# Optimization experiments

Measured on AMD Instinct MI355X. Metric: run time of the kernel, lower is better.

## Reference

```python
import jax, jax.numpy as jnp
import numpy as np


def setup_inputs() -> dict:
    key = jax.random.key(0)
    k1, k2, k3, k4 = jax.random.split(key, 4)
    B, T, C, H = 8, 2048, 1024, 64
    x = jax.random.normal(k1, (B, T, C), dtype=jnp.float32)
    # nn.Linear weights, stored as (in, out) for x @ W
    Wk = jax.random.normal(k2, (C, H), dtype=jnp.float32) * (C ** -0.5)
    Wq = jax.random.normal(k3, (C, H), dtype=jnp.float32) * (C ** -0.5)
    Wv = jax.random.normal(k4, (C, H), dtype=jnp.float32) * (C ** -0.5)
    return {"x": x, "Wk": Wk, "Wq": Wq, "Wv": Wv}


def reference(x, Wk, Wq, Wv):
    B, T, C = x.shape
    k = x @ Wk  # [B,T,H]
    q = x @ Wq  # [B,T,H]
    v = x @ Wv  # [B,T,H]
    # NOTE: original scales by C**-0.5 (full embed dim), not head_size**-0.5
    wei = jnp.einsum("bth,bsh->bts", q, k) * (C ** -0.5)  # [B,T,T]
    causal = jnp.tril(jnp.ones((T, T), dtype=bool))
    wei = jnp.where(causal, wei, -jnp.inf)
    wei = jax.nn.softmax(wei, axis=-1)
    # dropout is identity in eval/reference mode
    out = jnp.einsum("bts,bsh->bth", wei, v)  # [B,T,H]
    return out
```

## Files before the change

### kernel.cpp

```cpp
#include <hip/hip_runtime.h>
#include <hip/hip_bf16.h>
#include <math.h>

#define B_ 8
#define T_ 2048
#define C_ 1024
#define H_ 64
#define M_ (B_*T_)

typedef __attribute__((ext_vector_type(8))) short short8;
typedef __attribute__((ext_vector_type(4))) float f32x4;
typedef unsigned int u32;

__device__ __forceinline__ unsigned short f2bf(float f) {
    u32 u = __builtin_bit_cast(u32, f);
    u += 0x7FFFu + ((u >> 16) & 1u);
    return (unsigned short)(u >> 16);
}
__device__ __forceinline__ float bf2f(unsigned short h) {
    u32 u = ((u32)h) << 16;
    return __builtin_bit_cast(float, u);
}

__device__ __forceinline__ void gl2lds16(const void* g, void* l) {
    __builtin_amdgcn_global_load_lds(
        (const __attribute__((address_space(1))) u32*)g,
        (__attribute__((address_space(3))) u32*)l, 16, 0, 0);
}

__global__ __launch_bounds__(256) void wconv(
    const float* __restrict__ Wk, const float* __restrict__ Wq,
    const float* __restrict__ Wv, unsigned short* __restrict__ wb)
{
    __shared__ unsigned short lt[64][64];
    const int mat = blockIdx.x >> 4;
    const int k0  = (blockIdx.x & 15) * 64;
    const float* src = (mat == 0) ? Wk : (mat == 1 ? Wq : Wv);
    const float sc = (mat == 1) ? 0.03125f : 1.0f;
    const int tid = threadIdx.x;

    for (int it = 0; it < 16; ++it) {
        int idx = it * 256 + tid;
        int r = idx >> 6, cn = idx & 63;
        lt[cn][r] = f2bf(src[(size_t)(k0 + r) * H_ + cn] * sc);
    }
    __syncthreads();
    for (int g = 0; g < 2; ++g) {
        int n  = g * 32 + (tid >> 3);
        int kp = tid & 7;
        int ng = mat * 64 + n;
        short8 v = *reinterpret_cast<const short8*>(&lt[n][kp * 8]);
        char* dst = (char*)wb + (size_t)ng * 2048 + (k0 >> 6) * 128
                  + ((kp * 16) ^ ((ng & 7) << 4));
        *reinterpret_cast<short8*>(dst) = v;
    }
}

#define LOADX(R0,R1,R2,R3,t) {                                        \
    const float* p_ = xrow + (t) * 64;                                \
    R0 = *reinterpret_cast<const float4*>(p_);                        \
    R1 = *reinterpret_cast<const float4*>(p_ + 4);                    \
    R2 = *reinterpret_cast<const float4*>(p_ + 32);                   \
    R3 = *reinterpret_cast<const float4*>(p_ + 36); }

#define STAGEW(buf, t) {                                              \
    _Pragma("unroll") for (int p_ = 0; p_ < 6; ++p_) {                \
        int c_ = p_ * 256 + tid;                                      \
        gl2lds16((const char*)wb + (size_t)(c_ >> 3) * 2048           \
                     + (size_t)(t) * 128 + (c_ & 7) * 16,             \
                 (char*)&Ws[buf][0] + c_ * 16);                       \
    } }

__global__ __launch_bounds__(256) void qkv_mm(
    const float* __restrict__ x, const unsigned short* __restrict__ wb,
    unsigned short* __restrict__ kb, unsigned short* __restrict__ qb,
    unsigned short* __restrict__ vT)
{
    __shared__ __align__(16) unsigned short Ws[2][192 * 64];

    const int tid  = threadIdx.x;
    const int wid  = tid >> 6;
    const int lane = tid & 63;
    const int lr   = lane & 15;
    const int lg   = lane >> 4;
    const int m0   = blockIdx.x * 64;

    const float* xrow = x + (size_t)(m0 + wid * 16 + lr) * C_ + lg * 8;

    f32x4 acc[12];
    #pragma unroll
    for (int c = 0; c < 12; ++c) acc[c] = (f32x4){0.f, 0.f, 0.f, 0.f};

    float4 xA0, xA1, xA2, xA3, xB0, xB1, xB2, xB3, xC0, xC1, xC2, xC3;

    LOADX(xA0, xA1, xA2, xA3, 0);
    __builtin_amdgcn_sched_barrier(0);
    STAGEW(0, 0);
    __builtin_amdgcn_sched_barrier(0);
    LOADX(xB0, xB1, xB2, xB3, 1);
    __builtin_amdgcn_sched_barrier(0);

    #pragma unroll
    for (int t = 0; t < 16; ++t) {
        if (t < 15) asm volatile("s_waitcnt vmcnt(4) lgkmcnt(0)" ::: "memory");
        else        asm volatile("s_waitcnt vmcnt(0) lgkmcnt(0)" ::: "memory");
        __builtin_amdgcn_s_barrier();
        __builtin_amdgcn_sched_barrier(0);
        if (t < 15) { STAGEW((t + 1) & 1, t + 1); }
        __builtin_amdgcn_sched_barrier(0);
        if (t < 14) { LOADX(xC0, xC1, xC2, xC3, t + 2); }
        __builtin_amdgcn_sched_barrier(0);

        short8 af0, af1;
        af0[0] = (short)f2bf(xA0.x); af0[1] = (short)f2bf(xA0.y);
        af0[2] = (short)f2bf(xA0.z); af0[3] = (short)f2bf(xA0.w);
        af0[4] = (short)f2bf(xA1.x); af0[5] = (short)f2bf(xA1.y);
        af0[6] = (short)f2bf(xA1.z); af0[7] = (short)f2bf(xA1.w);
        af1[0] = (short)f2bf(xA2.x); af1[1] = (short)f2bf(xA2.y);
        af1[2] = (short)f2bf(xA2.z); af1[3] = (short)f2bf(xA2.w);
        af1[4] = (short)f2bf(xA3.x); af1[5] = (short)f2bf(xA3.y);
        af1[6] = (short)f2bf(xA3.z); af1[7] = (short)f2bf(xA3.w);

        const char* wbuf = (const char*)&Ws[t & 1][0];
        #pragma unroll
        for (int kc = 0; kc < 2; ++kc) {
            short8 afc = kc ? af1 : af0;
            #pragma unroll
            for (int ct = 0; ct < 12; ++ct) {
                int n = ct * 16 + lr;
                short8 bf = *reinterpret_cast<const short8*>(
                    wbuf + n * 128 + ((kc * 64 + lg * 16) ^ ((n & 7) << 4)));
                acc[ct] = __builtin_amdgcn_mfma_f32_16x16x32_bf16(afc, bf, acc[ct], 0, 0, 0);
            }
        }
        xA0 = xB0; xA1 = xB1; xA2 = xB2; xA3 = xB3;
        xB0 = xC0; xB1 = xC1; xB2 = xC2; xB3 = xC3;
    }

    #pragma unroll
    for (int ct = 0; ct < 12; ++ct) {
        int n = ct * 16 + lr;
        int col = n & 63;
        #pragma unroll
        for (int i = 0; i < 4; ++i) {
            int m = m0 + wid * 16 + lg * 4 + i;
            unsigned short val = f2bf(acc[ct][i]);
            if (n < 64)       kb[(size_t)m * H_ + col] = val;
            else if (n < 128) qb[(size_t)m * H_ + col] = val;
            else              vT[((size_t)(m >> 11) * H_ + col) * T_ + (m & (T_ - 1))] = val;
        }
    }
}

__global__ __launch_bounds__(64) void attn7(
    const unsigned short* __restrict__ kb,
    const unsigned short* __restrict__ qb,
    const unsigned short* __restrict__ vT,
    unsigned short* __restrict__ opart,
    float* __restrict__ ml)
{
    __shared__ __align__(16) unsigned short Ps[16][72];

    const int lane = threadIdx.x;
    const int lr   = lane & 15;
    const int lg   = lane >> 4;
    const int s0   = blockIdx.x;
    const int tile = 127 - blockIdx.y;
    const int b    = blockIdx.z;
    const int q0   = tile * 16;
    const int nst  = (tile >> 2) + 1;
    const size_t base = (size_t)b * T_ * H_;
    const unsigned short* vTb = vT + (size_t)b * H_ * T_;

    short8 qf[2];
    #pragma unroll
    for (int kc = 0; kc < 2; ++kc)
        qf[kc] = *reinterpret_cast<const short8*>(
            qb + base + (size_t)(q0 + lr) * H_ + kc * 32 + lg * 8);

    f32x4 o[4];
    float mrun[4], lrun[4];
    for (int dt = 0; dt < 4; ++dt) o[dt] = (f32x4){0.f, 0.f, 0.f, 0.f};
    for (int i = 0; i < 4; ++i) { mrun[i] = -INFINITY; lrun[i] = 0.f; }

    for (int s = s0; s < nst; s += 4) {
        const int kv0 = s * 64;

        f32x4 sv4[4];
        #pragma unroll
        for (int kt = 0; kt < 4; ++kt) sv4[kt] = (f32x4){0.f, 0.f, 0.f, 0.f};
        #pragma unroll
        for (int kc = 0; kc < 2; ++kc) {
            #pragma unroll
            for (int kt = 0; kt < 4; ++kt) {
                short8 kf = *reinterpret_cast<const short8*>(
                    kb + base + (size_t)(kv0 + kt * 16 + lr) * H_ + kc * 32 + lg * 8);
                sv4[kt] = __builtin_amdgcn_mfma_f32_16x16x32_bf16(qf[kc], kf, sv4[kt], 0, 0, 0);
            }
        }

        const bool need_mask = (s == nst - 1);
        #pragma unroll
        for (int i = 0; i < 4; ++i) {
            int row = q0 + lg * 4 + i;
            float sv[4];
            float mx = -INFINITY;
            if (need_mask) {
                #pragma unroll
                for (int kt = 0; kt < 4; ++kt) {
                    int key = kv0 + kt * 16 + lr;
                    float v = (key <= row) ? sv4[kt][i] : -INFINITY;
                    sv[kt] = v;
                    mx = fmaxf(mx, v);
                }
            } else {
                #pragma unroll
                for (int kt = 0; kt < 4; ++kt) {
                    sv[kt] = sv4[kt][i];
                    mx = fmaxf(mx, sv[kt]);
                }
            }
            for (int d = 8; d; d >>= 1) mx = fmaxf(mx, __shfl_xor(mx, d));
            float mn  = fmaxf(mrun[i], mx);
            float fac = __expf(mrun[i] - mn);
            float rs  = 0.f;
            #pragma unroll
            for (int kt = 0; kt < 4; ++kt) {
                float p = __expf(sv[kt] - mn);
                rs += p;
                Ps[lg * 4 + i][kt * 16 + lr] = f2bf(p);
            }
            for (int d = 8; d; d >>= 1) rs += __shfl_xor(rs, d);
            lrun[i] = lrun[i] * fac + rs;
            mrun[i] = mn;
            #pragma unroll
            for (int dt = 0; dt < 4; ++dt)
                o[dt][i] *= fac;
        }

        #pragma unroll
        for (int kc = 0; kc < 2; ++kc) {
            short8 pf = *reinterpret_cast<const short8*>(&Ps[lr][kc * 32 + lg * 8]);
            #pragma unroll
            for (int dt = 0; dt < 4; ++dt) {
                short8 vf = *reinterpret_cast<const short8*>(
                    vTb + (size_t)(dt * 16 + lr) * T_ + kv0 + kc * 32 + lg * 8);
                o[dt] = __builtin_amdgcn_mfma_f32_16x16x32_bf16(pf, vf, o[dt], 0, 0, 0);
            }
        }
    }

    unsigned short* op = opart + ((size_t)s0 * M_ + (size_t)b * T_ + q0) * H_;
    #pragma unroll
    for (int i = 0; i < 4; ++i)
        #pragma unroll
        for (int dt = 0; dt < 4; ++dt)
            op[(size_t)(lg * 4 + i) * H_ + dt * 16 + lr] = f2bf(o[dt][i]);
    if (lr == 0) {
        float* mlp = ml + ((size_t)s0 * M_ + (size_t)b * T_ + q0) * 2;
        #pragma unroll
        for (int i = 0; i < 4; ++i) {
            mlp[(lg * 4 + i) * 2 + 0] = mrun[i];
            mlp[(lg * 4 + i) * 2 + 1] = lrun[i];
        }
    }
}

__global__ __launch_bounds__(256) void attn_merge(
    const unsigned short* __restrict__ opart,
    const float* __restrict__ ml,
    float* __restrict__ out)
{
    const int idx = blockIdx.x * 256 + threadIdx.x;
    const int row = idx >> 6;
    const int col = idx & 63;

    float mv[4], lv[4];
    float M = -INFINITY;
    #pragma unroll
    for (int s = 0; s < 4; ++s) {
        mv[s] = ml[((size_t)s * M_ + row) * 2 + 0];
        lv[s] = ml[((size_t)s * M_ + row) * 2 + 1];
        M = fmaxf(M, mv[s]);
    }
    float L = 0.f, acc = 0.f;
    #pragma unroll
    for (int s = 0; s < 4; ++s) {
        float fac = __expf(mv[s] - M);
        L += lv[s] * fac;
        acc += bf2f(opart[(size_t)s * M_ * H_ + (size_t)row * H_ + col]) * fac;
    }
    out[idx] = acc / L;
}

extern "C" void kernel_launch(void* const* d_in, const int* in_sizes, int n_in,
                              void* d_out, int out_size, void* d_ws, size_t ws_size,
                              hipStream_t stream) {
    const float* x  = (const float*)d_in[0];
    const float* Wk = (const float*)d_in[1];
    const float* Wq = (const float*)d_in[2];
    const float* Wv = (const float*)d_in[3];
    float* out = (float*)d_out;

    unsigned short* kb    = (unsigned short*)d_ws;
    unsigned short* qb    = kb + (size_t)M_ * H_;
    unsigned short* vT    = qb + (size_t)M_ * H_;
    unsigned short* wb    = vT + (size_t)M_ * H_;
    unsigned short* opart = wb + (size_t)192 * C_;
    float*          ml    = (float*)(opart + (size_t)4 * M_ * H_);

    wconv<<<48, 256, 0, stream>>>(Wk, Wq, Wv, wb);
    qkv_mm<<<256, 256, 0, stream>>>(x, wb, kb, qb, vT);
    attn7<<<dim3(4, 128, B_), 64, 0, stream>>>(kb, qb, vT, opart, ml);
    attn_merge<<<M_ * H_ / 256, 256, 0, stream>>>(opart, ml, out);
}
```

Before: 162.8 us.

## Share K/V tiles across four query waves via double-buffered LDS; split QKV columns

The attention kernel now uses 256-thread blocks that cover 64 query rows (four waves). Each K/V tile is staged once into double-buffered, XOR-swizzled LDS with async global-to-LDS copies and shared by all four waves, where before every 64-thread block read K and V straight from global memory. The QKV projection kernel moves to 512 threads, with two wave groups each computing half of the 192 output columns, to raise occupancy and cut per-wave accumulator registers. The trade-off is block-wide barriers every KV step and coarser causal work granularity, since all four waves in a block now run the same number of KV steps.

```diff
diff --git a/kernel.cpp b/kernel.cpp
--- a/kernel.cpp
+++ b/kernel.cpp
@@ -64,14 +64,14 @@
     R3 = *reinterpret_cast<const float4*>(p_ + 36); }
 
 #define STAGEW(buf, t) {                                              \
-    _Pragma("unroll") for (int p_ = 0; p_ < 6; ++p_) {                \
-        int c_ = p_ * 256 + tid;                                      \
+    _Pragma("unroll") for (int p_ = 0; p_ < 3; ++p_) {                \
+        int c_ = p_ * 512 + tid;                                      \
         gl2lds16((const char*)wb + (size_t)(c_ >> 3) * 2048           \
                      + (size_t)(t) * 128 + (c_ & 7) * 16,             \
                  (char*)&Ws[buf][0] + c_ * 16);                       \
     } }
 
-__global__ __launch_bounds__(256) void qkv_mm(
+__global__ __launch_bounds__(512) void qkv_mm(
     const float* __restrict__ x, const unsigned short* __restrict__ wb,
     unsigned short* __restrict__ kb, unsigned short* __restrict__ qb,
     unsigned short* __restrict__ vT)
@@ -80,16 +80,18 @@
 
     const int tid  = threadIdx.x;
     const int wid  = tid >> 6;
+    const int rowg = wid & 3;
+    const int nh   = wid >> 2;
     const int lane = tid & 63;
     const int lr   = lane & 15;
     const int lg   = lane >> 4;
     const int m0   = blockIdx.x * 64;
 
-    const float* xrow = x + (size_t)(m0 + wid * 16 + lr) * C_ + lg * 8;
-
-    f32x4 acc[12];
-    #pragma unroll
-    for (int c = 0; c < 12; ++c) acc[c] = (f32x4){0.f, 0.f, 0.f, 0.f};
+    const float* xrow = x + (size_t)(m0 + rowg * 16 + lr) * C_ + lg * 8;
+
+    f32x4 acc[6];
+    #pragma unroll
+    for (int c = 0; c < 6; ++c) acc[c] = (f32x4){0.f, 0.f, 0.f, 0.f};
 
     float4 xA0, xA1, xA2, xA3, xB0, xB1, xB2, xB3, xC0, xC1, xC2, xC3;
 
@@ -126,8 +128,8 @@
         for (int kc = 0; kc < 2; ++kc) {
             short8 afc = kc ? af1 : af0;
             #pragma unroll
-            for (int ct = 0; ct < 12; ++ct) {
-                int n = ct * 16 + lr;
+            for (int ct = 0; ct < 6; ++ct) {
+                int n = nh * 96 + ct * 16 + lr;
                 short8 bf = *reinterpret_cast<const short8*>(
                     wbuf + n * 128 + ((kc * 64 + lg * 16) ^ ((n & 7) << 4)));
                 acc[ct] = __builtin_amdgcn_mfma_f32_16x16x32_bf16(afc, bf, acc[ct], 0, 0, 0);
@@ -138,12 +140,12 @@
     }
 
     #pragma unroll
-    for (int ct = 0; ct < 12; ++ct) {
-        int n = ct * 16 + lr;
+    for (int ct = 0; ct < 6; ++ct) {
+        int n = nh * 96 + ct * 16 + lr;
         int col = n & 63;
         #pragma unroll
         for (int i = 0; i < 4; ++i) {
-            int m = m0 + wid * 16 + lg * 4 + i;
+            int m = m0 + rowg * 16 + lg * 4 + i;
             unsigned short val = f2bf(acc[ct][i]);
             if (n < 64)       kb[(size_t)m * H_ + col] = val;
             else if (n < 128) qb[(size_t)m * H_ + col] = val;
@@ -152,40 +154,74 @@
     }
 }
 
-__global__ __launch_bounds__(64) void attn7(
+__global__ __launch_bounds__(256) void attn8(
     const unsigned short* __restrict__ kb,
     const unsigned short* __restrict__ qb,
     const unsigned short* __restrict__ vT,
     unsigned short* __restrict__ opart,
     float* __restrict__ ml)
 {
-    __shared__ __align__(16) unsigned short Ps[16][72];
-
-    const int lane = threadIdx.x;
+    __shared__ __align__(16) char KV[2][16384];
+    __shared__ __align__(16) unsigned short Ps[4][16][72];
+
+    const int tid  = threadIdx.x;
+    const int wid  = tid >> 6;
+    const int lane = tid & 63;
     const int lr   = lane & 15;
     const int lg   = lane >> 4;
     const int s0   = blockIdx.x;
-    const int tile = 127 - blockIdx.y;
+    const int tile = 31 - blockIdx.y;
     const int b    = blockIdx.z;
-    const int q0   = tile * 16;
-    const int nst  = (tile >> 2) + 1;
+    const int q0   = tile * 64;
+    const int wq0  = q0 + wid * 16;
+    const int nst  = tile + 1;
     const size_t base = (size_t)b * T_ * H_;
-    const unsigned short* vTb = vT + (size_t)b * H_ * T_;
+    const char* kbyte = (const char*)(kb + base);
+    const char* vbyte = (const char*)(vT + (size_t)b * H_ * T_);
+
+    auto STAGE = [&](int buf, int kv0) {
+        char* kd = KV[buf];
+        const char* ks = kbyte + (size_t)kv0 * 128;
+        const char* vs = vbyte + (size_t)kv0 * 2;
+        #pragma unroll
+        for (int i = 0; i < 2; ++i) {
+            int c = i * 256 + tid;
+            int row = c >> 3, colB = (c & 7) * 16;
+            gl2lds16(ks + row * 128 + (colB ^ ((row & 7) << 4)), kd + c * 16);
+        }
+        #pragma unroll
+        for (int i = 0; i < 2; ++i) {
+            int c = i * 256 + tid;
+            int row = c >> 3, colB = (c & 7) * 16;
+            gl2lds16(vs + (size_t)row * 4096 + (colB ^ ((row & 7) << 4)),
+                     kd + 8192 + c * 16);
+        }
+    };
 
     short8 qf[2];
     #pragma unroll
     for (int kc = 0; kc < 2; ++kc)
         qf[kc] = *reinterpret_cast<const short8*>(
-            qb + base + (size_t)(q0 + lr) * H_ + kc * 32 + lg * 8);
+            qb + base + (size_t)(wq0 + lr) * H_ + kc * 32 + lg * 8);
 
     f32x4 o[4];
     float mrun[4], lrun[4];
     for (int dt = 0; dt < 4; ++dt) o[dt] = (f32x4){0.f, 0.f, 0.f, 0.f};
     for (int i = 0; i < 4; ++i) { mrun[i] = -INFINITY; lrun[i] = 0.f; }
 
+    int cur = 0;
+    if (s0 < nst) STAGE(0, s0 * 64);
+
     for (int s = s0; s < nst; s += 4) {
         const int kv0 = s * 64;
-
+        const bool more = (s + 4) < nst;
+
+        asm volatile("s_waitcnt vmcnt(0)" ::: "memory");
+        __builtin_amdgcn_s_barrier();
+        __builtin_amdgcn_sched_barrier(0);
+        if (more) STAGE(cur ^ 1, kv0 + 256);
+
+        const char* kt_base = KV[cur];
         f32x4 sv4[4];
         #pragma unroll
         for (int kt = 0; kt < 4; ++kt) sv4[kt] = (f32x4){0.f, 0.f, 0.f, 0.f};
@@ -193,16 +229,17 @@
         for (int kc = 0; kc < 2; ++kc) {
             #pragma unroll
             for (int kt = 0; kt < 4; ++kt) {
+                int row = kt * 16 + lr;
                 short8 kf = *reinterpret_cast<const short8*>(
-                    kb + base + (size_t)(kv0 + kt * 16 + lr) * H_ + kc * 32 + lg * 8);
+                    kt_base + row * 128 + ((kc * 64 + lg * 16) ^ ((row & 7) << 4)));
                 sv4[kt] = __builtin_amdgcn_mfma_f32_16x16x32_bf16(qf[kc], kf, sv4[kt], 0, 0, 0);
             }
         }
 
-        const bool need_mask = (s == nst - 1);
+        const bool need_mask = (s == tile);
         #pragma unroll
         for (int i = 0; i < 4; ++i) {
-            int row = q0 + lg * 4 + i;
+            int row = wq0 + lg * 4 + i;
             float sv[4];
             float mx = -INFINITY;
             if (need_mask) {
@@ -228,7 +265,7 @@
             for (int kt = 0; kt < 4; ++kt) {
                 float p = __expf(sv[kt] - mn);
                 rs += p;
-                Ps[lg * 4 + i][kt * 16 + lr] = f2bf(p);
+                Ps[wid][lg * 4 + i][kt * 16 + lr] = f2bf(p);
             }
             for (int d = 8; d; d >>= 1) rs += __shfl_xor(rs, d);
             lrun[i] = lrun[i] * fac + rs;
@@ -238,26 +275,29 @@
                 o[dt][i] *= fac;
         }
 
+        const char* vt_base = KV[cur] + 8192;
         #pragma unroll
         for (int kc = 0; kc < 2; ++kc) {
-            short8 pf = *reinterpret_cast<const short8*>(&Ps[lr][kc * 32 + lg * 8]);
+            short8 pf = *reinterpret_cast<const short8*>(&Ps[wid][lr][kc * 32 + lg * 8]);
             #pragma unroll
             for (int dt = 0; dt < 4; ++dt) {
+                int row = dt * 16 + lr;
                 short8 vf = *reinterpret_cast<const short8*>(
-                    vTb + (size_t)(dt * 16 + lr) * T_ + kv0 + kc * 32 + lg * 8);
+                    vt_base + row * 128 + ((kc * 64 + lg * 16) ^ ((row & 7) << 4)));
                 o[dt] = __builtin_amdgcn_mfma_f32_16x16x32_bf16(pf, vf, o[dt], 0, 0, 0);
             }
         }
-    }
-
-    unsigned short* op = opart + ((size_t)s0 * M_ + (size_t)b * T_ + q0) * H_;
+        cur ^= 1;
+    }
+
+    unsigned short* op = opart + ((size_t)s0 * M_ + (size_t)b * T_ + wq0) * H_;
     #pragma unroll
     for (int i = 0; i < 4; ++i)
         #pragma unroll
         for (int dt = 0; dt < 4; ++dt)
             op[(size_t)(lg * 4 + i) * H_ + dt * 16 + lr] = f2bf(o[dt][i]);
     if (lr == 0) {
-        float* mlp = ml + ((size_t)s0 * M_ + (size_t)b * T_ + q0) * 2;
+        float* mlp = ml + ((size_t)s0 * M_ + (size_t)b * T_ + wq0) * 2;
         #pragma unroll
         for (int i = 0; i < 4; ++i) {
             mlp[(lg * 4 + i) * 2 + 0] = mrun[i];
@@ -310,7 +350,7 @@
     float*          ml    = (float*)(opart + (size_t)4 * M_ * H_);
 
     wconv<<<48, 256, 0, stream>>>(Wk, Wq, Wv, wb);
-    qkv_mm<<<256, 256, 0, stream>>>(x, wb, kb, qb, vT);
-    attn7<<<dim3(4, 128, B_), 64, 0, stream>>>(kb, qb, vT, opart, ml);
+    qkv_mm<<<256, 512, 0, stream>>>(x, wb, kb, qb, vT);
+    attn8<<<dim3(4, 32, B_), 256, 0, stream>>>(kb, qb, vT, opart, ml);
     attn_merge<<<M_ * H_ / 256, 256, 0, stream>>>(opart, ml, out);
 }
```

Result: faster. 155.8 us (-4.3%).
